# Performance work log

Measured on AMD Instinct MI355X. Metric: run time of the kernel, lower is better.

## Reference

```python
import jax, jax.numpy as jnp
import numpy as np
import math

CHUNK = 32
NS_STEPS = 5
MAX_GNORM = 10.0


def _normalize(x, eps=1e-12):
    n = jnp.linalg.norm(x, axis=-1, keepdims=True)
    return x / jnp.maximum(n, eps)


def _poly(x):  # poly_degree = 2: [x, x^2] / sqrt(2)
    return jnp.concatenate([x, x * x], axis=-1) / math.sqrt(2.0)


def _ns5(G):
    # Muon-style Newton-Schulz orthogonalization (quintic, 5 steps)
    a, b, c = 3.4445, -4.7750, 2.0315
    t = G.shape[0] > G.shape[1]
    X = G.T if t else G
    X = X / (jnp.linalg.norm(X) + 1e-7)
    for _ in range(NS_STEPS):
        A = X @ X.T
        B = b * A + c * (A @ A)
        X = a * X + B @ X
    return X.T if t else X


def _clip_mean(g):
    # per-sample grad-norm clipping to MAX_GNORM, then mean over samples
    n = g.shape[0]
    norms = jnp.maximum(jnp.linalg.norm(g.reshape(n, -1), axis=1), 1e-8)
    scale = jnp.maximum(norms / MAX_GNORM, 1.0)
    return jnp.mean(g / scale.reshape((n,) + (1,) * (g.ndim - 1)), axis=0)


def _mem_fwd(W0, W1, z):  # MemoryMLP depth=2, gelu (exact) between layers
    return jax.nn.gelu(z @ W0, approximate=False) @ W1


def setup_inputs() -> dict:
    key = jax.random.key(0)
    ks = jax.random.split(key, 16)
    B, S, D, M, P, H = 2, 1024, 2048, 512, 1024, 2048
    w = lambda k, shape, fan_in: jax.random.normal(k, shape, jnp.float32) / np.float32(np.sqrt(fan_in))
    return {
        "x": jax.random.normal(ks[0], (B, S, D), jnp.float32),
        "Wk": w(ks[1], (M, D), D),
        "Wv": w(ks[2], (M, D), D),
        "Wq": w(ks[3], (M, D), D),
        "Wout": w(ks[4], (D, M), M),
        "w_lr": w(ks[5], (1, D), D), "b_lr": jnp.full((1,), -4.0, jnp.float32),
        "w_mom": w(ks[6], (1, D), D), "b_mom": jnp.full((1,), 1.0, jnp.float32),
        "w_dec": w(ks[7], (1, D), D), "b_dec": jnp.full((1,), -3.0, jnp.float32),
        "w_gate": w(ks[8], (1, D), D), "b_gate": jnp.full((1,), -1.0, jnp.float32),
        "Wmem0": w(ks[9], (P, H), P),
        "Wmem1": w(ks[10], (H, P), H),
        "Wmemout": w(ks[11], (P, M), P),
        "Wvexp": w(ks[12], (M, P), M),
    }


def reference(x, Wk, Wv, Wq, Wout, w_lr, b_lr, w_mom, b_mom, w_dec, b_dec,
              w_gate, b_gate, Wmem0, Wmem1, Wmemout, Wvexp):
    # Inference path (torch.is_grad_enabled() == False): chunked ATLAS update.
    B, S, D = x.shape
    NC = S // CHUNK

    k = _normalize(x @ Wk.T)          # (B,S,M)
    v = x @ Wv.T                       # (B,S,M)
    q = _normalize(x @ Wq.T)          # (B,S,M)
    kp = _poly(k)                      # (B,S,P)
    qp = _poly(q)                      # (B,S,P)
    vexp = v @ Wvexp                   # v_expand: (B,S,P)

    gate = lambda w, b: jax.nn.sigmoid(jnp.einsum('bsd,od->bso', x, w) + b)
    lr, mom, dec, og = gate(w_lr, b_lr), gate(w_mom, b_mom), gate(w_dec, b_dec), gate(w_gate, b_gate)

    cmean = lambda t: t[..., 0].reshape(B, NC, CHUNK).mean(axis=(0, 2))  # per-chunk scalar
    lr_c, mom_c, dec_c = cmean(lr), cmean(mom), cmean(dec)

    chunks = lambda t: t.reshape(B, NC, CHUNK, t.shape[-1]).transpose(1, 0, 2, 3)  # (NC,B,C,F)
    qc, kc, vc = chunks(qp), chunks(kp), chunks(vexp)

    def loss_fn(params, kk, vv):  # ||M(k) - v||^2 per sample
        W0_, W1_ = params
        pred = jax.nn.gelu(kk @ W0_, approximate=False) @ W1_
        return jnp.sum((pred - vv) ** 2)

    grad_fn = jax.vmap(jax.grad(loss_fn), in_axes=((None, None), 0, 0))

    def step(carry, xs):
        W0, W1, S0, S1 = carry
        qch, kch, vch, lrc, momc, decc = xs
        retr = _mem_fwd(W0, W1, qch) @ Wmemout  # retrieve with pre-update params: (B,C,M)
        kf = kch.reshape(-1, kch.shape[-1])
        vf = vch.reshape(-1, vch.shape[-1])
        g0, g1 = grad_fn((W0, W1), kf, vf)      # per-sample grads
        g0, g1 = _clip_mean(g0), _clip_mean(g1)
        s0 = momc * S0 - lrc * g0                # surprise momentum
        s1 = momc * S1 - lrc * g1
        W0n = (1.0 - decc) * W0 + _ns5(s0) * lrc # forget gate + orthogonalized step
        W1n = (1.0 - decc) * W1 + _ns5(s1) * lrc
        return (W0n, W1n, s0, s1), retr

    init = (Wmem0, Wmem1, jnp.zeros_like(Wmem0), jnp.zeros_like(Wmem1))
    _, retrs = jax.lax.scan(step, init, (qc, kc, vc, lr_c, mom_c, dec_c))
    retrieved = retrs.transpose(1, 0, 2, 3).reshape(B, S, -1)  # (B,S,M)
    delta = retrieved @ Wout.T
    return x + delta * og
```

## Files before the change

kernel.cpp:

```cpp
#include <hip/hip_runtime.h>


typedef unsigned short us;
typedef __attribute__((ext_vector_type(8))) short s16x8;
typedef __attribute__((ext_vector_type(8))) unsigned short u16x8;
typedef __attribute__((ext_vector_type(4))) float f32x4;

#define MKP 72

__device__ __forceinline__ float gelu_f(float x) {
  return 0.5f * x * (1.0f + erff(x * 0.70710678118654752f));
}
__device__ __forceinline__ float gelu_grad_f(float x) {
  float cdf = 0.5f * (1.0f + erff(x * 0.70710678118654752f));
  float pdf = 0.3989422804014327f * expf(-0.5f * x * x);
  return cdf + x * pdf;
}
__device__ __forceinline__ float sigmoid_f(float x) { return 1.0f / (1.0f + expf(-x)); }

__device__ __forceinline__ us f2bf(float f) {
  union { float f; unsigned u; } v; v.f = f;
  unsigned r = (v.u + 0x7FFFu + ((v.u >> 16) & 1u)) >> 16;
  return (us)r;
}
__device__ __forceinline__ float bf2f(us h) {
  union { unsigned u; float f; } v; v.u = ((unsigned)h) << 16;
  return v.f;
}
__device__ __forceinline__ int cm_map(int n) {
  return ((n & 1023) >> 5) * 64 + (n >> 10) * 32 + (n & 31);
}

__device__ __forceinline__ float block_reduce_sum(float v, float* red) {
  int t = threadIdx.x;
  red[t] = v; __syncthreads();
  for (int s = blockDim.x >> 1; s > 0; s >>= 1) {
    if (t < s) red[t] += red[t + s];
    __syncthreads();
  }
  float r = red[0];
  __syncthreads();
  return r;
}

template<int EPI, int TA, int DUAL, int AG>
__global__ __launch_bounds__(64)
void mg_k(const us* __restrict__ Aq, const us* __restrict__ A2,
          const us* __restrict__ Bq, void* __restrict__ Cq,
          void* __restrict__ C2, const void* __restrict__ Eq,
          const float* __restrict__ FX, const float* __restrict__ OG,
          const float* __restrict__ cp, int cidx,
          int M, int N, int K, int lda, int ldb, int ldc, int lde,
          float c1, float c2, long sA, long sB, long sC, long sE) {
  __shared__ __align__(16) us As[64 * MKP];
  __shared__ __align__(16) us Bs[64 * MKP];
  const int bz = blockIdx.z;
  const us* A = Aq + (size_t)bz * sA;
  const us* B = Bq + (size_t)bz * sB;
  const int t = threadIdx.x;
  const int m0 = blockIdx.y * 64, n0 = blockIdx.x * 64;
  if constexpr (DUAL) { if (m0 >= 64) A = A2; }
  const int mA0 = DUAL ? (m0 & 63) : m0;
  const int l15 = t & 15, l4 = t >> 4;

  f32x4 acc[4][4];
#pragma unroll
  for (int i = 0; i < 4; ++i)
#pragma unroll
    for (int j = 0; j < 4; ++j) acc[i][j] = (f32x4){0.f, 0.f, 0.f, 0.f};

  const int srw = t >> 3;
  const int sck = (t & 7) * 8;

  u16x8 ra[8], rb[8];
  auto LDA = [&](int k0) {
#pragma unroll
    for (int p = 0; p < 8; ++p) {
      if constexpr (TA == 0) {
        int row = srw + p * 8;
        int srow;
        if constexpr (AG) srow = cm_map(m0 + row); else srow = mA0 + row;
        ra[p] = *(const u16x8*)(A + (size_t)srow * lda + k0 + sck);
      } else {
        ra[p] = *(const u16x8*)(A + (size_t)(k0 + srw + p * 8) * lda + mA0 + sck);
      }
    }
  };
  auto LDB = [&](int k0) {
#pragma unroll
    for (int p = 0; p < 8; ++p)
      rb[p] = *(const u16x8*)(B + (size_t)(n0 + srw + p * 8) * ldb + k0 + sck);
  };

  LDA(0); LDB(0);
  for (int k0 = 0; k0 < K; k0 += 64) {
    if constexpr (TA == 0) {
#pragma unroll
      for (int p = 0; p < 8; ++p)
        *(u16x8*)&As[(srw + p * 8) * MKP + sck] = ra[p];
    } else {
#pragma unroll
      for (int p = 0; p < 8; ++p) {
        int kk = srw + p * 8;
#pragma unroll
        for (int j = 0; j < 8; ++j) As[(sck + j) * MKP + kk] = ra[p][j];
      }
    }
#pragma unroll
    for (int p = 0; p < 8; ++p)
      *(u16x8*)&Bs[(srw + p * 8) * MKP + sck] = rb[p];
    if (k0 + 64 < K) { LDA(k0 + 64); LDB(k0 + 64); }
#pragma unroll
    for (int ks = 0; ks < 2; ++ks) {
      s16x8 af[4], bf[4];
#pragma unroll
      for (int mi = 0; mi < 4; ++mi)
        af[mi] = *(const s16x8*)&As[(mi * 16 + l15) * MKP + ks * 32 + l4 * 8];
#pragma unroll
      for (int ni = 0; ni < 4; ++ni)
        bf[ni] = *(const s16x8*)&Bs[(ni * 16 + l15) * MKP + ks * 32 + l4 * 8];
#pragma unroll
      for (int mi = 0; mi < 4; ++mi)
#pragma unroll
        for (int ni = 0; ni < 4; ++ni)
          acc[mi][ni] = __builtin_amdgcn_mfma_f32_16x16x32_bf16(af[mi], bf[ni], acc[mi][ni], 0, 0, 0);
    }
  }

#pragma unroll
  for (int mi = 0; mi < 4; ++mi) {
#pragma unroll
    for (int i = 0; i < 4; ++i) {
      int grow = m0 + mi * 16 + l4 * 4 + i;
#pragma unroll
      for (int ni = 0; ni < 4; ++ni) {
        int col = n0 + ni * 16 + l15;
        float v = acc[mi][ni][i];
        if constexpr (EPI == 5) {
          ((us*)Cq + bz * sC)[(size_t)grow * ldc + col] = f2bf(v);
        } else if constexpr (EPI == 6) {
          const us* E = (const us*)Eq + bz * sE;
          ((us*)Cq + bz * sC)[(size_t)grow * ldc + col] =
              f2bf(c1 * v + c2 * bf2f(E[(size_t)grow * lde + col]));
        } else if constexpr (EPI == 7) {
          ((float*)Cq)[(size_t)grow * ldc + col] = v;
        } else if constexpr (EPI == 8) {
          ((us*)Cq)[(size_t)grow * ldc + col] = f2bf(gelu_f(v));
          if (m0 >= 64)
            ((float*)C2)[(size_t)(grow - 64) * ldc + col] = gelu_grad_f(v);
        } else if constexpr (EPI == 9) {
          if (m0 < 64)
            ((us*)Cq)[(size_t)grow * ldc + col] = f2bf(v);
          else
            ((us*)Cq)[(size_t)grow * ldc + col] =
                f2bf(2.0f * (v - ((const float*)Eq)[(size_t)(grow - 64) * lde + col]));
        } else if constexpr (EPI == 13) {
          ((float*)Cq)[(size_t)grow * ldc + col] =
              v * ((const float*)Eq)[(size_t)grow * lde + col];
        } else if constexpr (EPI == 14) {
          float* C = (float*)Cq;
          float old = C[(size_t)grow * ldc + col];
          C[(size_t)grow * ldc + col] = cp[cidx * 3 + 1] * old - cp[cidx * 3 + 0] * v;
        } else if constexpr (EPI == 15) {
          ((float*)Cq)[(size_t)grow * ldc + col] =
              FX[(size_t)grow * ldc + col] + v * OG[grow];
        } else if constexpr (EPI == 17) {
          int crow = cm_map(grow);
          ((float*)Cq)[(size_t)crow * ldc + col] = v;
        }
      }
    }
  }
}

template<int EPI, int TA = 0, int DUAL = 0, int AG = 0>
static void mg(hipStream_t st, const us* A, const us* A2, const us* B,
               void* C, void* C2, const void* E,
               const float* FX, const float* OG, const float* cp, int cidx,
               int M, int N, int K, int lda, int ldb, int ldc, int lde,
               float c1, float c2, long sA, long sB, long sC, long sE, int batch) {
  dim3 g(N / 64, M / 64, batch), b(64);
  hipLaunchKernelGGL((mg_k<EPI, TA, DUAL, AG>), g, b, 0, st, A, A2, B, C, C2, E,
                     FX, OG, cp, cidx, M, N, K, lda, ldb, ldc, lde, c1, c2, sA, sB, sC, sE);
}


__global__ __launch_bounds__(256) void conv_k(const float* __restrict__ in,
                                              us* __restrict__ out, int n) {
  for (int i = blockIdx.x * 256 + threadIdx.x; i < n; i += gridDim.x * 256)
    out[i] = f2bf(in[i]);
}

__global__ void tconv_k(const float* __restrict__ in, us* __restrict__ out, int R, int C) {
  __shared__ float tile[32][33];
  int c0 = blockIdx.x * 32, r0 = blockIdx.y * 32;
  int tx = threadIdx.x, ty = threadIdx.y;
#pragma unroll
  for (int j = 0; j < 4; ++j)
    tile[ty + 8 * j][tx] = in[(size_t)(r0 + ty + 8 * j) * C + c0 + tx];
  __syncthreads();
#pragma unroll
  for (int j = 0; j < 4; ++j)
    out[(size_t)(c0 + ty + 8 * j) * R + r0 + tx] = f2bf(tile[tx][ty + 8 * j]);
}


__global__ __launch_bounds__(256) void polynorm2_k(const float* __restrict__ lin,
                                                   us* __restrict__ outp) {
  __shared__ float red[256];
  int n = blockIdx.x, t = threadIdx.x;
  int rowp = cm_map(n);
  float s = 0.f;
  for (int f = t; f < 512; f += 256) { float v = lin[(size_t)n * 512 + f]; s += v * v; }
  float tot = block_reduce_sum(s, red);
  float sc = 1.0f / fmaxf(sqrtf(tot), 1e-12f);
  const float is2 = 0.70710678118654752f;
  for (int f = t; f < 512; f += 256) {
    float v = lin[(size_t)n * 512 + f] * sc;
    outp[(size_t)rowp * 1024 + f] = f2bf(v * is2);
    outp[(size_t)rowp * 1024 + 512 + f] = f2bf(v * v * is2);
  }
}

__global__ __launch_bounds__(256) void gates_k(const float* __restrict__ x,
    const float* __restrict__ wlr, const float* __restrict__ blr,
    const float* __restrict__ wmom, const float* __restrict__ bmom,
    const float* __restrict__ wdec, const float* __restrict__ bdec,
    const float* __restrict__ wgate, const float* __restrict__ bgate,
    float* __restrict__ lrv, float* __restrict__ momv,
    float* __restrict__ decv, float* __restrict__ og) {
  __shared__ float red[256];
  int n = blockIdx.x, t = threadIdx.x;
  float s0 = 0.f, s1 = 0.f, s2 = 0.f, s3 = 0.f;
  for (int d = t; d < 2048; d += 256) {
    float xv = x[(size_t)n * 2048 + d];
    s0 += xv * wlr[d]; s1 += xv * wmom[d]; s2 += xv * wdec[d]; s3 += xv * wgate[d];
  }
  float r0 = block_reduce_sum(s0, red);
  float r1 = block_reduce_sum(s1, red);
  float r2 = block_reduce_sum(s2, red);
  float r3 = block_reduce_sum(s3, red);
  if (t == 0) {
    lrv[n] = sigmoid_f(r0 + blr[0]);
    momv[n] = sigmoid_f(r1 + bmom[0]);
    decv[n] = sigmoid_f(r2 + bdec[0]);
    og[n] = sigmoid_f(r3 + bgate[0]);
  }
}

__global__ void chunk_means_k(const float* __restrict__ lrv, const float* __restrict__ momv,
                              const float* __restrict__ decv, float* __restrict__ cp) {
  int c = blockIdx.x, t = threadIdx.x;
  int n = ((t >> 5) << 10) + c * 32 + (t & 31);
  float a = lrv[n], b = momv[n], d = decv[n];
  for (int off = 32; off > 0; off >>= 1) {
    a += __shfl_down(a, off);
    b += __shfl_down(b, off);
    d += __shfl_down(d, off);
  }
  if (t == 0) {
    cp[c * 3 + 0] = a * (1.f / 64.f);
    cp[c * 3 + 1] = b * (1.f / 64.f);
    cp[c * 3 + 2] = d * (1.f / 64.f);
  }
}

__global__ __launch_bounds__(256) void sampnorm2_k(const us* __restrict__ kp_b,
                                                   const float* __restrict__ dh,
                                                   const us* __restrict__ hab,
                                                   const us* __restrict__ pr,
                                                   float* __restrict__ w0inv,
                                                   float* __restrict__ w1inv, int c) {
  __shared__ float red[256];
  int i = blockIdx.x, t = threadIdx.x;
  int row = c * 64 + i;
  float sk = 0.f, sr = 0.f, sdh = 0.f, sa = 0.f;
  for (int p = t; p < 1024; p += 256) {
    float v = bf2f(kp_b[(size_t)row * 1024 + p]); sk += v * v;
    v = bf2f(pr[(size_t)(64 + i) * 1024 + p]); sr += v * v;
  }
  for (int h = t; h < 2048; h += 256) {
    float v = dh[(size_t)i * 2048 + h]; sdh += v * v;
    v = bf2f(hab[(size_t)(64 + i) * 2048 + h]); sa += v * v;
  }
  float tk = block_reduce_sum(sk, red);
  float tdh = block_reduce_sum(sdh, red);
  float ta = block_reduce_sum(sa, red);
  float tr = block_reduce_sum(sr, red);
  if (t == 0) {
    float n0 = fmaxf(sqrtf(tk) * sqrtf(tdh), 1e-8f);
    w0inv[i] = 1.0f / (64.0f * fmaxf(n0 * 0.1f, 1.0f));
    float n1 = fmaxf(sqrtf(ta) * sqrtf(tr), 1e-8f);
    w1inv[i] = 1.0f / (64.0f * fmaxf(n1 * 0.1f, 1.0f));
  }
}

template<int INF32>
__global__ void wtrans_k(const void* __restrict__ in, const float* __restrict__ w,
                         us* __restrict__ out, int C, int ldin) {
  __shared__ float tile[32][33];
  int c0 = blockIdx.x * 32, r0 = blockIdx.y * 32;
  int tx = threadIdx.x, ty = threadIdx.y;
#pragma unroll
  for (int j = 0; j < 4; ++j) {
    int r = r0 + ty + 8 * j, cc = c0 + tx;
    float v;
    if constexpr (INF32) v = ((const float*)in)[(size_t)r * ldin + cc];
    else v = bf2f(((const us*)in)[(size_t)r * ldin + cc]);
    tile[ty + 8 * j][tx] = v * w[r];
  }
  __syncthreads();
#pragma unroll
  for (int j = 0; j < 4; ++j)
    out[(size_t)(c0 + ty + 8 * j) * 64 + r0 + tx] = f2bf(tile[tx][ty + 8 * j]);
}

__global__ __launch_bounds__(256) void frob2_k(const float* __restrict__ s0,
                                               const float* __restrict__ s1, int n,
                                               float* __restrict__ parts) {
  __shared__ float red[256];
  const float* s = blockIdx.z ? s1 : s0;
  float acc = 0.f;
  for (int i = blockIdx.x * 256 + threadIdx.x; i < n; i += gridDim.x * 256) {
    float v = s[i]; acc += v * v;
  }
  float r = block_reduce_sum(acc, red);
  if (threadIdx.x == 0) parts[blockIdx.z * 256 + blockIdx.x] = r;
}

__global__ __launch_bounds__(256) void frob_fin2_k(const float* __restrict__ parts,
                                                   float* __restrict__ inv) {
  __shared__ float red[256];
  float r = block_reduce_sum(parts[blockIdx.x * 256 + threadIdx.x], red);
  if (threadIdx.x == 0) inv[blockIdx.x] = 1.0f / (sqrtf(r) + 1e-7f);
}

__global__ void scale_dual_k(const float* __restrict__ in, us* __restrict__ outS,
                             us* __restrict__ outT, const float* __restrict__ inv,
                             int R, int C) {
  __shared__ float tile[32][33];
  float s = *inv;
  int c0 = blockIdx.x * 32, r0 = blockIdx.y * 32;
  int tx = threadIdx.x, ty = threadIdx.y;
#pragma unroll
  for (int j = 0; j < 4; ++j) {
    float v = in[(size_t)(r0 + ty + 8 * j) * C + c0 + tx];
    tile[ty + 8 * j][tx] = v;
    outS[(size_t)(r0 + ty + 8 * j) * C + c0 + tx] = f2bf(v * s);
  }
  __syncthreads();
#pragma unroll
  for (int j = 0; j < 4; ++j)
    outT[(size_t)(c0 + ty + 8 * j) * R + r0 + tx] = f2bf(tile[tx][ty + 8 * j] * s);
}

__global__ void tbf_k(const us* __restrict__ in, us* __restrict__ out) {
  __shared__ us tile[32][33];
  size_t bo = (size_t)blockIdx.z * 2097152;
  int c0 = blockIdx.x * 32, r0 = blockIdx.y * 32;
  int tx = threadIdx.x, ty = threadIdx.y;
#pragma unroll
  for (int j = 0; j < 4; ++j)
    tile[ty + 8 * j][tx] = in[bo + (size_t)(r0 + ty + 8 * j) * 2048 + c0 + tx];
  __syncthreads();
#pragma unroll
  for (int j = 0; j < 4; ++j)
    out[bo + (size_t)(c0 + ty + 8 * j) * 1024 + r0 + tx] = tile[tx][ty + 8 * j];
}

__global__ void wupd0_k(float* __restrict__ W0, const us* __restrict__ X,
                        us* __restrict__ W0bT, const float* __restrict__ cp, int c) {
  __shared__ float tl[32][33];
  float lr = cp[c * 3 + 0], om = 1.0f - cp[c * 3 + 2];
  int c0 = blockIdx.x * 32, r0 = blockIdx.y * 32;
  int tx = threadIdx.x, ty = threadIdx.y;
#pragma unroll
  for (int j = 0; j < 4; ++j) {
    int r = r0 + ty + 8 * j, h = c0 + tx;
    size_t idx = (size_t)r * 2048 + h;
    float v = om * W0[idx] + lr * bf2f(X[idx]);
    W0[idx] = v;
    tl[ty + 8 * j][tx] = v;
  }
  __syncthreads();
#pragma unroll
  for (int j = 0; j < 4; ++j)
    W0bT[(size_t)(c0 + ty + 8 * j) * 1024 + r0 + tx] = f2bf(tl[tx][ty + 8 * j]);
}

__global__ void wupd1_k(float* __restrict__ W1, const us* __restrict__ X2,
                        us* __restrict__ W1b, us* __restrict__ W1bT,
                        const float* __restrict__ cp, int c) {
  __shared__ float tX[32][33];
  __shared__ float t2[32][33];
  float lr = cp[c * 3 + 0], om = 1.0f - cp[c * 3 + 2];
  int h0 = blockIdx.x * 32, p0 = blockIdx.y * 32;
  int tx = threadIdx.x, ty = threadIdx.y;
#pragma unroll
  for (int j = 0; j < 4; ++j)
    tX[ty + 8 * j][tx] = bf2f(X2[(size_t)(p0 + ty + 8 * j) * 2048 + h0 + tx]);
  __syncthreads();
#pragma unroll
  for (int j = 0; j < 4; ++j) {
    int h = h0 + ty + 8 * j, p = p0 + tx;
    size_t idx = (size_t)h * 1024 + p;
    float v = om * W1[idx] + lr * tX[tx][ty + 8 * j];
    W1[idx] = v;
    W1b[idx] = f2bf(v);
    t2[tx][ty + 8 * j] = v;
  }
  __syncthreads();
#pragma unroll
  for (int j = 0; j < 4; ++j)
    W1bT[(size_t)(p0 + ty + 8 * j) * 2048 + h0 + tx] = f2bf(t2[ty + 8 * j][tx]);
}


extern "C" void kernel_launch(void* const* d_in, const int* in_sizes, int n_in,
                              void* d_out, int out_size, void* d_ws, size_t ws_size,
                              hipStream_t stream) {
  const float* x = (const float*)d_in[0];
  const float* Wk = (const float*)d_in[1];
  const float* Wv = (const float*)d_in[2];
  const float* Wq = (const float*)d_in[3];
  const float* Wout = (const float*)d_in[4];
  const float* w_lr = (const float*)d_in[5];
  const float* b_lr = (const float*)d_in[6];
  const float* w_mom = (const float*)d_in[7];
  const float* b_mom = (const float*)d_in[8];
  const float* w_dec = (const float*)d_in[9];
  const float* b_dec = (const float*)d_in[10];
  const float* w_gate = (const float*)d_in[11];
  const float* b_gate = (const float*)d_in[12];
  const float* Wmem0 = (const float*)d_in[13];
  const float* Wmem1 = (const float*)d_in[14];
  const float* Wmemout = (const float*)d_in[15];
  const float* Wvexp = (const float*)d_in[16];
  float* out = (float*)d_out;
  (void)n_in; (void)in_sizes; (void)out_size;

  const long F = 1048576;
  const long BIG = 2097152;
  const long SB2 = 2097152, SB1 = 1048576;
  float* ws = (float*)d_ws;
  if (ws_size < (size_t)25043464 * sizeof(float)) return;

  us* kp_b   = (us*)ws;
  us* qp_b   = (us*)(ws + F);
  float* vexp = ws + 2 * F;
  float* W0  = ws + 4 * F;
  float* W1  = ws + 6 * F;
  float* S0  = ws + 8 * F;
  float* S1  = ws + 10 * F;
  us* XA     = (us*)(ws + 12 * F);
  us* XB     = (us*)(ws + 14 * F);
  us* XT     = (us*)(ws + 16 * F);
  us* Ab     = (us*)(ws + 18 * F);
  float* SCR = ws + 19 * F;
  us* W0bT   = (us*)(ws + 20 * F);
  us* W1bT   = (us*)(ws + 21 * F);
  us* W1b    = (us*)(ws + 22 * F);
  us* WmoT   = (us*)(ws + 23 * F);
  us* retrv  = (us*)(ws + 23 * F + 262144);
  float* smal = ws + 23 * F + 262144 + 524288;
  float* og   = smal;
  float* lrv  = og + 2048;
  float* momv = lrv + 2048;
  float* decv = momv + 2048;
  float* cpb  = decv + 2048;
  float* w0inv = cpb + 128;
  float* w1inv = w0inv + 64;
  float* parts = w1inv + 64;
  float* inv01 = parts + 512;

  us* xb   = XA;
  us* Wkb  = XB;
  us* Wqb  = XB + 1048576;
  us* Wvb  = XB + 2097152;
  us* vlin = XT;
  us* WvexpT = XT + 1048576;
  us* Woutb = Ab;
  float* lin = SCR;
  us* Bb = (us*)SCR;
  us* hab   = (us*)SCR;
  float* gp = SCR + 131072;
  us* pr    = (us*)(SCR + 262144);
  float* dh = SCR + 327680;
  us* dhT   = (us*)(SCR + 458752);
  us* rbwT  = (us*)(SCR + 524288);

  const float NSa = 3.4445f, NSb = -4.7750f, NSc = 2.0315f;

  hipMemcpyAsync(W0, Wmem0, (size_t)BIG * 4, hipMemcpyDeviceToDevice, stream);
  hipMemcpyAsync(W1, Wmem1, (size_t)BIG * 4, hipMemcpyDeviceToDevice, stream);
  hipMemsetAsync(S0, 0, (size_t)BIG * 4, stream);
  hipMemsetAsync(S1, 0, (size_t)BIG * 4, stream);
  hipLaunchKernelGGL(tconv_k, dim3(64, 32), dim3(32, 8), 0, stream, Wmem0, W0bT, 1024, 2048);
  hipLaunchKernelGGL(conv_k, dim3(1024), dim3(256), 0, stream, Wmem1, W1b, (int)BIG);
  hipLaunchKernelGGL(tconv_k, dim3(32, 64), dim3(32, 8), 0, stream, Wmem1, W1bT, 2048, 1024);
  hipLaunchKernelGGL(tconv_k, dim3(16, 32), dim3(32, 8), 0, stream, Wmemout, WmoT, 1024, 512);
  hipLaunchKernelGGL(tconv_k, dim3(32, 16), dim3(32, 8), 0, stream, Wvexp, WvexpT, 512, 1024);
  hipLaunchKernelGGL(conv_k, dim3(2048), dim3(256), 0, stream, x, xb, 2048 * 2048);
  hipLaunchKernelGGL(conv_k, dim3(512), dim3(256), 0, stream, Wk, Wkb, 512 * 2048);
  hipLaunchKernelGGL(conv_k, dim3(512), dim3(256), 0, stream, Wq, Wqb, 512 * 2048);
  hipLaunchKernelGGL(conv_k, dim3(512), dim3(256), 0, stream, Wv, Wvb, 512 * 2048);

  mg<7>(stream, xb, nullptr, Wkb, lin, nullptr, nullptr, nullptr, nullptr, nullptr, 0,
        2048, 512, 2048, 2048, 2048, 512, 0, 0.f, 0.f, 0, 0, 0, 0, 1);
  hipLaunchKernelGGL(polynorm2_k, dim3(2048), dim3(256), 0, stream, lin, kp_b);
  mg<7>(stream, xb, nullptr, Wqb, lin, nullptr, nullptr, nullptr, nullptr, nullptr, 0,
        2048, 512, 2048, 2048, 2048, 512, 0, 0.f, 0.f, 0, 0, 0, 0, 1);
  hipLaunchKernelGGL(polynorm2_k, dim3(2048), dim3(256), 0, stream, lin, qp_b);
  mg<5>(stream, xb, nullptr, Wvb, vlin, nullptr, nullptr, nullptr, nullptr, nullptr, 0,
        2048, 512, 2048, 2048, 2048, 512, 0, 0.f, 0.f, 0, 0, 0, 0, 1);
  mg<17>(stream, vlin, nullptr, WvexpT, vexp, nullptr, nullptr, nullptr, nullptr, nullptr, 0,
         2048, 1024, 512, 512, 512, 1024, 0, 0.f, 0.f, 0, 0, 0, 0, 1);

  hipLaunchKernelGGL(gates_k, dim3(2048), dim3(256), 0, stream, x,
                     w_lr, b_lr, w_mom, b_mom, w_dec, b_dec, w_gate, b_gate,
                     lrv, momv, decv, og);
  hipLaunchKernelGGL(chunk_means_k, dim3(32), dim3(64), 0, stream, lrv, momv, decv, cpb);

  for (int c = 0; c < 32; ++c) {
    const us* kp_c = kp_b + (size_t)c * 64 * 1024;
    const us* qp_c = qp_b + (size_t)c * 64 * 1024;
    const float* vexp_c = vexp + (size_t)c * 64 * 1024;
    mg<8, 0, 1>(stream, qp_c, kp_c, W0bT, hab, gp, nullptr, nullptr, nullptr, nullptr, 0,
                128, 2048, 1024, 1024, 1024, 2048, 0, 0.f, 0.f, 0, 0, 0, 0, 1);
    mg<9>(stream, hab, nullptr, W1bT, pr, nullptr, vexp_c, nullptr, nullptr, nullptr, 0,
          128, 1024, 2048, 2048, 2048, 1024, 1024, 0.f, 0.f, 0, 0, 0, 0, 1);
    mg<5>(stream, pr, nullptr, WmoT, retrv + (size_t)c * 64 * 512, nullptr, nullptr,
          nullptr, nullptr, nullptr, 0,
          64, 512, 1024, 1024, 1024, 512, 0, 0.f, 0.f, 0, 0, 0, 0, 1);
    mg<13>(stream, pr + 64 * 1024, nullptr, W1b, dh, nullptr, gp, nullptr, nullptr, nullptr, 0,
           64, 2048, 1024, 1024, 1024, 2048, 2048, 0.f, 0.f, 0, 0, 0, 0, 1);
    hipLaunchKernelGGL(sampnorm2_k, dim3(64), dim3(256), 0, stream,
                       kp_b, dh, hab, pr, w0inv, w1inv, c);
    hipLaunchKernelGGL((wtrans_k<1>), dim3(64, 2), dim3(32, 8), 0, stream, dh, w0inv, dhT, 2048, 2048);
    hipLaunchKernelGGL((wtrans_k<0>), dim3(32, 2), dim3(32, 8), 0, stream, pr + 64 * 1024, w1inv,
                       rbwT, 1024, 1024);
    mg<14, 1>(stream, kp_c, nullptr, dhT, S0, nullptr, nullptr, nullptr, nullptr, cpb, c,
              1024, 2048, 64, 1024, 64, 2048, 0, 0.f, 0.f, 0, 0, 0, 0, 1);
    mg<14, 1>(stream, hab + 64 * 2048, nullptr, rbwT, S1, nullptr, nullptr, nullptr, nullptr, cpb, c,
              2048, 1024, 64, 2048, 64, 1024, 0, 0.f, 0.f, 0, 0, 0, 0, 1);

    hipLaunchKernelGGL(frob2_k, dim3(256, 1, 2), dim3(256), 0, stream, S0, S1, (int)BIG, parts);
    hipLaunchKernelGGL(frob_fin2_k, dim3(2), dim3(256), 0, stream, parts, inv01);
    hipLaunchKernelGGL(scale_dual_k, dim3(64, 32), dim3(32, 8), 0, stream,
                       S0, XA, XT, inv01, 1024, 2048);
    hipLaunchKernelGGL(scale_dual_k, dim3(32, 64), dim3(32, 8), 0, stream,
                       S1, XT + SB2, XA + SB2, inv01 + 1, 2048, 1024);

    us* Xc = XA;
    us* Xn = XB;
    for (int it = 0; it < 5; ++it) {
      mg<5>(stream, Xc, nullptr, Xc, Ab, nullptr, nullptr, nullptr, nullptr, nullptr, 0,
            1024, 1024, 2048, 2048, 2048, 1024, 0, 0.f, 0.f, SB2, SB2, SB1, 0, 2);
      mg<6>(stream, Ab, nullptr, Ab, Bb, nullptr, Ab, nullptr, nullptr, nullptr, 0,
            1024, 1024, 1024, 1024, 1024, 1024, 1024, NSc, NSb, SB1, SB1, SB1, SB1, 2);
      mg<6>(stream, Bb, nullptr, XT, Xn, nullptr, Xc, nullptr, nullptr, nullptr, 0,
            1024, 2048, 1024, 1024, 1024, 2048, 2048, 1.0f, NSa, SB1, SB2, SB2, SB2, 2);
      if (it < 4)
        hipLaunchKernelGGL(tbf_k, dim3(64, 32, 2), dim3(32, 8), 0, stream, Xn, XT);
      us* tmp = Xc; Xc = Xn; Xn = tmp;
    }
    hipLaunchKernelGGL(wupd0_k, dim3(64, 32), dim3(32, 8), 0, stream, W0, Xc, W0bT, cpb, c);
    hipLaunchKernelGGL(wupd1_k, dim3(64, 32), dim3(32, 8), 0, stream, W1, Xc + SB2, W1b, W1bT, cpb, c);
  }

  hipLaunchKernelGGL(conv_k, dim3(1024), dim3(256), 0, stream, Wout, Woutb, 2048 * 512);
  mg<15, 0, 0, 1>(stream, retrv, nullptr, Woutb, out, nullptr, nullptr, x, og, nullptr, 0,
                  2048, 2048, 512, 512, 512, 2048, 0, 0.f, 0.f, 0, 0, 0, 0, 1);
}
```

Baseline: 16.89 ms.

## Use 128x128 LDS-direct GEMM with split-K for Newton-Schulz iterations

Adds a new 256-thread GEMM kernel with 128x128 tiles, swizzled shared memory and direct global-to-LDS loads, and uses it for the three Newton-Schulz matmuls. The two square products (X X^T and A A) are split along K into two partial results, which are then summed by small elementwise combine kernels. This is meant to raise occupancy on the 1024x1024 outputs and improve data reuse compared with the 64x64 single-wave kernel. In exchange it adds extra kernel launches and memory traffic for the partials, and bf16 partial sums add rounding error.

```diff
diff --git a/kernel.cpp b/kernel.cpp
--- a/kernel.cpp
+++ b/kernel.cpp
@@ -29,6 +29,12 @@
 }
 __device__ __forceinline__ int cm_map(int n) {
   return ((n & 1023) >> 5) * 64 + (n >> 10) * 32 + (n & 31);
+}
+
+__device__ __forceinline__ void gload16(const us* g, us* l) {
+  __builtin_amdgcn_global_load_lds(
+      (const __attribute__((address_space(1))) void*)g,
+      (__attribute__((address_space(3))) void*)l, 16, 0, 0);
 }
 
 __device__ __forceinline__ float block_reduce_sum(float v, float* red) {
@@ -41,6 +47,125 @@
   float r = red[0];
   __syncthreads();
   return r;
+}
+
+template<int KS, int EPI>
+__global__ __launch_bounds__(256)
+void ns_k(const us* __restrict__ Aq, const us* __restrict__ Bq,
+          us* __restrict__ Cq, const us* __restrict__ Eq,
+          int M, int N, int K, int lda, int ldb, int ldc, int lde,
+          float c1, float c2, long sA, long sB, long sC, long sE) {
+  __shared__ __align__(16) us As[128 * 64];
+  __shared__ __align__(16) us Bs[128 * 64];
+  const int bz = blockIdx.z;
+  const int bb = bz / KS, ss = bz % KS;
+  const int KH = K / KS;
+  const us* A = Aq + (size_t)bb * sA + (size_t)ss * KH;
+  const us* B = Bq + (size_t)bb * sB + (size_t)ss * KH;
+  us* C = Cq + (size_t)bz * sC;
+  const int t = threadIdx.x;
+  const int wave = t >> 6, lane = t & 63;
+  const int m0 = blockIdx.y * 128, n0 = blockIdx.x * 128;
+  const int wm = (wave >> 1) * 64, wn = (wave & 1) * 64;
+  const int l15 = lane & 15, l4 = lane >> 4;
+  const int lr = lane >> 3;
+  const int lu = lane & 7;
+
+  f32x4 acc[4][4];
+#pragma unroll
+  for (int i = 0; i < 4; ++i)
+#pragma unroll
+    for (int j = 0; j < 4; ++j) acc[i][j] = (f32x4){0.f, 0.f, 0.f, 0.f};
+
+  for (int k0 = 0; k0 < KH; k0 += 64) {
+#pragma unroll
+    for (int j = 0; j < 4; ++j) {
+      int r = (wave * 4 + j) * 8 + lr;
+      int u = lu ^ (r & 7);
+      gload16(A + (size_t)(m0 + r) * lda + k0 + u * 8, As + (wave * 4 + j) * 512);
+      gload16(B + (size_t)(n0 + r) * ldb + k0 + u * 8, Bs + (wave * 4 + j) * 512);
+    }
+    __syncthreads();
+#pragma unroll
+    for (int ks = 0; ks < 2; ++ks) {
+      s16x8 af[4], bf[4];
+#pragma unroll
+      for (int mi = 0; mi < 4; ++mi) {
+        int ra = wm + mi * 16 + l15;
+        int cu = (ks * 4 + l4) ^ (ra & 7);
+        af[mi] = *(const s16x8*)&As[ra * 64 + cu * 8];
+      }
+#pragma unroll
+      for (int ni = 0; ni < 4; ++ni) {
+        int rb = wn + ni * 16 + l15;
+        int cu = (ks * 4 + l4) ^ (rb & 7);
+        bf[ni] = *(const s16x8*)&Bs[rb * 64 + cu * 8];
+      }
+#pragma unroll
+      for (int mi = 0; mi < 4; ++mi)
+#pragma unroll
+        for (int ni = 0; ni < 4; ++ni)
+          acc[mi][ni] = __builtin_amdgcn_mfma_f32_16x16x32_bf16(af[mi], bf[ni], acc[mi][ni], 0, 0, 0);
+    }
+    __syncthreads();
+  }
+
+#pragma unroll
+  for (int mi = 0; mi < 4; ++mi) {
+#pragma unroll
+    for (int i = 0; i < 4; ++i) {
+      int row = m0 + wm + mi * 16 + l4 * 4 + i;
+#pragma unroll
+      for (int ni = 0; ni < 4; ++ni) {
+        int col = n0 + wn + ni * 16 + l15;
+        float v = acc[mi][ni][i];
+        if constexpr (EPI == 0) {
+          C[(size_t)row * ldc + col] = f2bf(v);
+        } else {
+          const us* E = Eq + (size_t)bb * sE;
+          C[(size_t)row * ldc + col] =
+              f2bf(c1 * v + c2 * bf2f(E[(size_t)row * lde + col]));
+        }
+      }
+    }
+  }
+}
+
+template<int KS, int EPI>
+static void nsg(hipStream_t st, const us* A, const us* B, us* C, const us* E,
+                int M, int N, int K, int lda, int ldb, int ldc, int lde,
+                float c1, float c2, long sA, long sB, long sC, long sE, int batch) {
+  dim3 g(N / 128, M / 128, batch * KS), b(256);
+  hipLaunchKernelGGL((ns_k<KS, EPI>), g, b, 0, st, A, B, C, E,
+                     M, N, K, lda, ldb, ldc, lde, c1, c2, sA, sB, sC, sE);
+}
+
+__global__ __launch_bounds__(256) void combA_k(const u16x8* __restrict__ P,
+                                               u16x8* __restrict__ Ab) {
+  int i = blockIdx.x * 256 + threadIdx.x;
+  int b = i >> 17, j = i & 131071;
+  u16x8 p0 = P[(size_t)(b * 2) * 131072 + j];
+  u16x8 p1 = P[(size_t)(b * 2 + 1) * 131072 + j];
+  u16x8 o;
+#pragma unroll
+  for (int q = 0; q < 8; ++q) o[q] = f2bf(bf2f(p0[q]) + bf2f(p1[q]));
+  Ab[i] = o;
+}
+
+__global__ __launch_bounds__(256) void combB_k(const u16x8* __restrict__ P,
+                                               const u16x8* __restrict__ Ab,
+                                               u16x8* __restrict__ Bb,
+                                               float nsb, float nsc) {
+  int i = blockIdx.x * 256 + threadIdx.x;
+  int b = i >> 17, j = i & 131071;
+  u16x8 p0 = P[(size_t)(b * 2) * 131072 + j];
+  u16x8 p1 = P[(size_t)(b * 2 + 1) * 131072 + j];
+  u16x8 ab = Ab[i];
+  u16x8 o;
+#pragma unroll
+  for (int q = 0; q < 8; ++q)
+    o[q] = f2bf(nsc * (bf2f(p0[q]) + bf2f(p1[q])) + nsb * bf2f(ab[q]));
+  Bb[i] = o;
 }
 
 template<int EPI, int TA, int DUAL, int AG>
@@ -138,10 +263,6 @@
         float v = acc[mi][ni][i];
         if constexpr (EPI == 5) {
           ((us*)Cq + bz * sC)[(size_t)grow * ldc + col] = f2bf(v);
-        } else if constexpr (EPI == 6) {
-          const us* E = (const us*)Eq + bz * sE;
-          ((us*)Cq + bz * sC)[(size_t)grow * ldc + col] =
-              f2bf(c1 * v + c2 * bf2f(E[(size_t)grow * lde + col]));
         } else if constexpr (EPI == 7) {
           ((float*)Cq)[(size_t)grow * ldc + col] = v;
         } else if constexpr (EPI == 8) {
@@ -554,12 +675,17 @@
     us* Xc = XA;
     us* Xn = XB;
     for (int it = 0; it < 5; ++it) {
-      mg<5>(stream, Xc, nullptr, Xc, Ab, nullptr, nullptr, nullptr, nullptr, nullptr, 0,
-            1024, 1024, 2048, 2048, 2048, 1024, 0, 0.f, 0.f, SB2, SB2, SB1, 0, 2);
-      mg<6>(stream, Ab, nullptr, Ab, Bb, nullptr, Ab, nullptr, nullptr, nullptr, 0,
-            1024, 1024, 1024, 1024, 1024, 1024, 1024, NSc, NSb, SB1, SB1, SB1, SB1, 2);
-      mg<6>(stream, Bb, nullptr, XT, Xn, nullptr, Xc, nullptr, nullptr, nullptr, 0,
-            1024, 2048, 1024, 1024, 1024, 2048, 2048, 1.0f, NSa, SB1, SB2, SB2, SB2, 2);
+      us* P = Xn;
+      nsg<2, 0>(stream, Xc, Xc, P, nullptr, 1024, 1024, 2048, 2048, 2048, 1024, 0,
+                0.f, 0.f, SB2, SB2, SB1, 0, 2);
+      hipLaunchKernelGGL(combA_k, dim3(1024), dim3(256), 0, stream,
+                         (const u16x8*)P, (u16x8*)Ab);
+      nsg<2, 0>(stream, Ab, Ab, P, nullptr, 1024, 1024, 1024, 1024, 1024, 1024, 0,
+                0.f, 0.f, SB1, SB1, SB1, 0, 2);
+      hipLaunchKernelGGL(combB_k, dim3(1024), dim3(256), 0, stream,
+                         (const u16x8*)P, (const u16x8*)Ab, (u16x8*)Bb, NSb, NSc);
+      nsg<1, 6>(stream, Bb, XT, Xn, Xc, 1024, 2048, 1024, 1024, 1024, 2048, 2048,
+                1.0f, NSa, SB1, SB2, SB2, SB2, 2);
       if (it < 4)
         hipLaunchKernelGGL(tbf_k, dim3(64, 32, 2), dim3(32, 8), 0, stream, Xn, XT);
       us* tmp = Xc; Xc = Xn; Xn = tmp;
```

After: 17.79 ms. 1.05x slower.

## Split-K the Newton-Schulz GEMMs and fuse combine with transpose

Applied to the files above, without the earlier changes.

Each of the three Newton-Schulz GEMMs per iteration is split into two K halves, doubling the block count to improve CU occupancy on the small 64-thread-block grid. The partial bf16 results are summed by new combine kernels that also apply the polynomial coefficients. The final combine fuses the transpose previously done by tbf_k. This adds extra partial-sum traffic and kernel launches, reuses scratch buffers such as W0bT, and rounds the partials to bf16 before summing, which slightly changes precision.

```diff
diff --git a/kernel.cpp b/kernel.cpp
--- a/kernel.cpp
+++ b/kernel.cpp
@@ -43,90 +43,11 @@
   return r;
 }
 
-template<int EPI, int TA, int DUAL, int AG>
-__global__ __launch_bounds__(64)
-void mg_k(const us* __restrict__ Aq, const us* __restrict__ A2,
-          const us* __restrict__ Bq, void* __restrict__ Cq,
-          void* __restrict__ C2, const void* __restrict__ Eq,
-          const float* __restrict__ FX, const float* __restrict__ OG,
-          const float* __restrict__ cp, int cidx,
-          int M, int N, int K, int lda, int ldb, int ldc, int lde,
-          float c1, float c2, long sA, long sB, long sC, long sE) {
-  __shared__ __align__(16) us As[64 * MKP];
-  __shared__ __align__(16) us Bs[64 * MKP];
-  const int bz = blockIdx.z;
-  const us* A = Aq + (size_t)bz * sA;
-  const us* B = Bq + (size_t)bz * sB;
-  const int t = threadIdx.x;
-  const int m0 = blockIdx.y * 64, n0 = blockIdx.x * 64;
-  if constexpr (DUAL) { if (m0 >= 64) A = A2; }
-  const int mA0 = DUAL ? (m0 & 63) : m0;
-  const int l15 = t & 15, l4 = t >> 4;
-
-  f32x4 acc[4][4];
-#pragma unroll
-  for (int i = 0; i < 4; ++i)
-#pragma unroll
-    for (int j = 0; j < 4; ++j) acc[i][j] = (f32x4){0.f, 0.f, 0.f, 0.f};
-
-  const int srw = t >> 3;
-  const int sck = (t & 7) * 8;
-
-  u16x8 ra[8], rb[8];
-  auto LDA = [&](int k0) {
-#pragma unroll
-    for (int p = 0; p < 8; ++p) {
-      if constexpr (TA == 0) {
-        int row = srw + p * 8;
-        int srow;
-        if constexpr (AG) srow = cm_map(m0 + row); else srow = mA0 + row;
-        ra[p] = *(const u16x8*)(A + (size_t)srow * lda + k0 + sck);
-      } else {
-        ra[p] = *(const u16x8*)(A + (size_t)(k0 + srw + p * 8) * lda + mA0 + sck);
-      }
-    }
-  };
-  auto LDB = [&](int k0) {
-#pragma unroll
-    for (int p = 0; p < 8; ++p)
-      rb[p] = *(const u16x8*)(B + (size_t)(n0 + srw + p * 8) * ldb + k0 + sck);
-  };
-
-  LDA(0); LDB(0);
-  for (int k0 = 0; k0 < K; k0 += 64) {
-    if constexpr (TA == 0) {
-#pragma unroll
-      for (int p = 0; p < 8; ++p)
-        *(u16x8*)&As[(srw + p * 8) * MKP + sck] = ra[p];
-    } else {
-#pragma unroll
-      for (int p = 0; p < 8; ++p) {
-        int kk = srw + p * 8;
-#pragma unroll
-        for (int j = 0; j < 8; ++j) As[(sck + j) * MKP + kk] = ra[p][j];
-      }
-    }
-#pragma unroll
-    for (int p = 0; p < 8; ++p)
-      *(u16x8*)&Bs[(srw + p * 8) * MKP + sck] = rb[p];
-    if (k0 + 64 < K) { LDA(k0 + 64); LDB(k0 + 64); }
-#pragma unroll
-    for (int ks = 0; ks < 2; ++ks) {
-      s16x8 af[4], bf[4];
-#pragma unroll
-      for (int mi = 0; mi < 4; ++mi)
-        af[mi] = *(const s16x8*)&As[(mi * 16 + l15) * MKP + ks * 32 + l4 * 8];
-#pragma unroll
-      for (int ni = 0; ni < 4; ++ni)
-        bf[ni] = *(const s16x8*)&Bs[(ni * 16 + l15) * MKP + ks * 32 + l4 * 8];
-#pragma unroll
-      for (int mi = 0; mi < 4; ++mi)
-#pragma unroll
-        for (int ni = 0; ni < 4; ++ni)
-          acc[mi][ni] = __builtin_amdgcn_mfma_f32_16x16x32_bf16(af[mi], bf[ni], acc[mi][ni], 0, 0, 0);
-    }
-  }
-
+template<int EPI>
+__device__ __forceinline__ void epilogue(f32x4 (&acc)[4][4], int m0, int n0,
+    int l15, int l4, void* Cq, void* C2, const void* Eq,
+    const float* FX, const float* OG, const float* cp, int cidx,
+    int ldc, int lde, float c1, float c2) {
 #pragma unroll
   for (int mi = 0; mi < 4; ++mi) {
 #pragma unroll
@@ -137,11 +58,10 @@
         int col = n0 + ni * 16 + l15;
         float v = acc[mi][ni][i];
         if constexpr (EPI == 5) {
-          ((us*)Cq + bz * sC)[(size_t)grow * ldc + col] = f2bf(v);
+          ((us*)Cq)[(size_t)grow * ldc + col] = f2bf(v);
         } else if constexpr (EPI == 6) {
-          const us* E = (const us*)Eq + bz * sE;
-          ((us*)Cq + bz * sC)[(size_t)grow * ldc + col] =
-              f2bf(c1 * v + c2 * bf2f(E[(size_t)grow * lde + col]));
+          ((us*)Cq)[(size_t)grow * ldc + col] =
+              f2bf(c1 * v + c2 * bf2f(((const us*)Eq)[(size_t)grow * lde + col]));
         } else if constexpr (EPI == 7) {
           ((float*)Cq)[(size_t)grow * ldc + col] = v;
         } else if constexpr (EPI == 8) {
@@ -173,15 +93,176 @@
   }
 }
 
-template<int EPI, int TA = 0, int DUAL = 0, int AG = 0>
+template<int EPI, int TA, int DUAL, int AG, int KS>
+__global__ __launch_bounds__(64)
+void mg_k(const us* __restrict__ Aq, const us* __restrict__ A2,
+          const us* __restrict__ Bq, void* __restrict__ Cq,
+          void* __restrict__ C2, const void* __restrict__ Eq,
+          const float* __restrict__ FX, const float* __restrict__ OG,
+          const float* __restrict__ cp, int cidx,
+          int M, int N, int K, int lda, int ldb, int ldc, int lde,
+          float c1, float c2, long sA, long sB, long sC, long sE, int zthr) {
+  __shared__ __align__(16) us As[64 * MKP];
+  __shared__ __align__(16) us Bs[64 * MKP];
+  const int bz = blockIdx.z;
+  const int bb = bz / KS, ss = bz % KS;
+  const int KH = K / KS;
+  const us* A = Aq + (size_t)bb * sA;
+  if constexpr (TA == 0) A += (size_t)ss * KH;
+  else A += (size_t)ss * KH * lda;
+  const us* B = Bq + (size_t)bb * sB + (size_t)ss * KH;
+  const int t = threadIdx.x;
+  const int m0 = blockIdx.y * 64, n0 = blockIdx.x * 64;
+  if constexpr (DUAL) { if (m0 >= 64) A = A2; }
+  const int mA0 = DUAL ? (m0 & 63) : m0;
+  const int l15 = t & 15, l4 = t >> 4;
+
+  f32x4 acc[4][4];
+#pragma unroll
+  for (int i = 0; i < 4; ++i)
+#pragma unroll
+    for (int j = 0; j < 4; ++j) acc[i][j] = (f32x4){0.f, 0.f, 0.f, 0.f};
+
+  const int srw = t >> 3;
+  const int sck = (t & 7) * 8;
+
+  u16x8 ra[8], rb[8];
+  auto LDA = [&](int k0) {
+#pragma unroll
+    for (int p = 0; p < 8; ++p) {
+      if constexpr (TA == 0) {
+        int row = srw + p * 8;
+        int srow;
+        if constexpr (AG) srow = cm_map(m0 + row); else srow = mA0 + row;
+        ra[p] = *(const u16x8*)(A + (size_t)srow * lda + k0 + sck);
+      } else {
+        ra[p] = *(const u16x8*)(A + (size_t)(k0 + srw + p * 8) * lda + mA0 + sck);
+      }
+    }
+  };
+  auto LDB = [&](int k0) {
+#pragma unroll
+    for (int p = 0; p < 8; ++p)
+      rb[p] = *(const u16x8*)(B + (size_t)(n0 + srw + p * 8) * ldb + k0 + sck);
+  };
+
+  LDA(0); LDB(0);
+  for (int k0 = 0; k0 < KH; k0 += 64) {
+    if constexpr (TA == 0) {
+#pragma unroll
+      for (int p = 0; p < 8; ++p)
+        *(u16x8*)&As[(srw + p * 8) * MKP + sck] = ra[p];
+    } else {
+#pragma unroll
+      for (int p = 0; p < 8; ++p) {
+        int kk = srw + p * 8;
+#pragma unroll
+        for (int j = 0; j < 8; ++j) As[(sck + j) * MKP + kk] = ra[p][j];
+      }
+    }
+#pragma unroll
+    for (int p = 0; p < 8; ++p)
+      *(u16x8*)&Bs[(srw + p * 8) * MKP + sck] = rb[p];
+    if (k0 + 64 < KH) { LDA(k0 + 64); LDB(k0 + 64); }
+#pragma unroll
+    for (int ks = 0; ks < 2; ++ks) {
+      s16x8 af[4], bf[4];
+#pragma unroll
+      for (int mi = 0; mi < 4; ++mi)
+        af[mi] = *(const s16x8*)&As[(mi * 16 + l15) * MKP + ks * 32 + l4 * 8];
+#pragma unroll
+      for (int ni = 0; ni < 4; ++ni)
+        bf[ni] = *(const s16x8*)&Bs[(ni * 16 + l15) * MKP + ks * 32 + l4 * 8];
+#pragma unroll
+      for (int mi = 0; mi < 4; ++mi)
+#pragma unroll
+        for (int ni = 0; ni < 4; ++ni)
+          acc[mi][ni] = __builtin_amdgcn_mfma_f32_16x16x32_bf16(af[mi], bf[ni], acc[mi][ni], 0, 0, 0);
+    }
+  }
+
+  if constexpr (EPI == 5 || EPI == 6) {
+    void* Cb; long cb;
+    if (bz < zthr) { Cb = Cq; cb = bz; } else { Cb = C2; cb = bz - zthr; }
+    us* Cp = (us*)Cb + (size_t)cb * sC;
+    const us* Ep = (const us*)Eq + (size_t)bb * sE;
+    epilogue<EPI>(acc, m0, n0, l15, l4, Cp, nullptr, Ep, FX, OG, cp, cidx,
+                  ldc, lde, c1, c2);
+  } else {
+    epilogue<EPI>(acc, m0, n0, l15, l4, Cq, C2, Eq, FX, OG, cp, cidx,
+                  ldc, lde, c1, c2);
+  }
+}
+
+template<int EPI, int TA = 0, int DUAL = 0, int AG = 0, int KS = 1>
 static void mg(hipStream_t st, const us* A, const us* A2, const us* B,
                void* C, void* C2, const void* E,
                const float* FX, const float* OG, const float* cp, int cidx,
                int M, int N, int K, int lda, int ldb, int ldc, int lde,
-               float c1, float c2, long sA, long sB, long sC, long sE, int batch) {
-  dim3 g(N / 64, M / 64, batch), b(64);
-  hipLaunchKernelGGL((mg_k<EPI, TA, DUAL, AG>), g, b, 0, st, A, A2, B, C, C2, E,
-                     FX, OG, cp, cidx, M, N, K, lda, ldb, ldc, lde, c1, c2, sA, sB, sC, sE);
+               float c1, float c2, long sA, long sB, long sC, long sE,
+               int batch, int zthr = (1 << 30)) {
+  dim3 g(N / 64, M / 64, batch * KS), b(64);
+  hipLaunchKernelGGL((mg_k<EPI, TA, DUAL, AG, KS>), g, b, 0, st, A, A2, B, C, C2, E,
+                     FX, OG, cp, cidx, M, N, K, lda, ldb, ldc, lde, c1, c2,
+                     sA, sB, sC, sE, zthr);
+}
+
+
+__global__ __launch_bounds__(256) void combA_k(const u16x8* __restrict__ P,
+                                               u16x8* __restrict__ Ab) {
+  int i = blockIdx.x * 256 + threadIdx.x;
+  int b = i >> 17, j = i & 131071;
+  u16x8 p0 = P[(size_t)(b * 2) * 131072 + j];
+  u16x8 p1 = P[(size_t)(b * 2 + 1) * 131072 + j];
+  u16x8 o;
+#pragma unroll
+  for (int q = 0; q < 8; ++q) o[q] = f2bf(bf2f(p0[q]) + bf2f(p1[q]));
+  Ab[i] = o;
+}
+
+__global__ __launch_bounds__(256) void combB_k(const u16x8* __restrict__ P,
+                                               const u16x8* __restrict__ Ab,
+                                               u16x8* __restrict__ Bb,
+                                               float nsb, float nsc) {
+  int i = blockIdx.x * 256 + threadIdx.x;
+  int b = i >> 17, j = i & 131071;
+  u16x8 p0 = P[(size_t)(b * 2) * 131072 + j];
+  u16x8 p1 = P[(size_t)(b * 2 + 1) * 131072 + j];
+  u16x8 ab = Ab[i];
+  u16x8 o;
+#pragma unroll
+  for (int q = 0; q < 8; ++q)
+    o[q] = f2bf(nsc * (bf2f(p0[q]) + bf2f(p1[q])) + nsb * bf2f(ab[q]));
+  Bb[i] = o;
+}
+
+__global__ void combX_k(const us* __restrict__ P0, const us* __restrict__ P1,
+                        const us* __restrict__ Xc, us* __restrict__ Xn,
+                        us* __restrict__ XT, float nsa, int doT) {
+  __shared__ us tile[32][33];
+  const long SB2c = 2097152;
+  int b = blockIdx.z;
+  int h0 = blockIdx.x * 32, r0 = blockIdx.y * 32;
+  int tx = threadIdx.x, ty = threadIdx.y;
+  const us* pa = (b * 2 == 0) ? P0 : P1 + (size_t)(b * 2 - 1) * SB2c;
+  const us* pb = P1 + (size_t)(b * 2) * SB2c;
+  const us* xc = Xc + (size_t)b * SB2c;
+  us* xn = Xn + (size_t)b * SB2c;
+  us* xt = XT + (size_t)b * SB2c;
+#pragma unroll
+  for (int j = 0; j < 4; ++j) {
+    size_t idx = (size_t)(r0 + ty + 8 * j) * 2048 + h0 + tx;
+    float v = bf2f(pa[idx]) + bf2f(pb[idx]) + nsa * bf2f(xc[idx]);
+    us uv = f2bf(v);
+    xn[idx] = uv;
+    tile[ty + 8 * j][tx] = uv;
+  }
+  __syncthreads();
+  if (doT) {
+#pragma unroll
+    for (int j = 0; j < 4; ++j)
+      xt[(size_t)(h0 + ty + 8 * j) * 1024 + r0 + tx] = tile[tx][ty + 8 * j];
+  }
 }
 
 
@@ -352,20 +433,6 @@
 #pragma unroll
   for (int j = 0; j < 4; ++j)
     outT[(size_t)(c0 + ty + 8 * j) * R + r0 + tx] = f2bf(tile[tx][ty + 8 * j] * s);
-}
-
-__global__ void tbf_k(const us* __restrict__ in, us* __restrict__ out) {
-  __shared__ us tile[32][33];
-  size_t bo = (size_t)blockIdx.z * 2097152;
-  int c0 = blockIdx.x * 32, r0 = blockIdx.y * 32;
-  int tx = threadIdx.x, ty = threadIdx.y;
-#pragma unroll
-  for (int j = 0; j < 4; ++j)
-    tile[ty + 8 * j][tx] = in[bo + (size_t)(r0 + ty + 8 * j) * 2048 + c0 + tx];
-  __syncthreads();
-#pragma unroll
-  for (int j = 0; j < 4; ++j)
-    out[bo + (size_t)(c0 + ty + 8 * j) * 1024 + r0 + tx] = tile[tx][ty + 8 * j];
 }
 
 __global__ void wupd0_k(float* __restrict__ W0, const us* __restrict__ X,
@@ -554,14 +621,25 @@
     us* Xc = XA;
     us* Xn = XB;
     for (int it = 0; it < 5; ++it) {
-      mg<5>(stream, Xc, nullptr, Xc, Ab, nullptr, nullptr, nullptr, nullptr, nullptr, 0,
-            1024, 1024, 2048, 2048, 2048, 1024, 0, 0.f, 0.f, SB2, SB2, SB1, 0, 2);
-      mg<6>(stream, Ab, nullptr, Ab, Bb, nullptr, Ab, nullptr, nullptr, nullptr, 0,
-            1024, 1024, 1024, 1024, 1024, 1024, 1024, NSc, NSb, SB1, SB1, SB1, SB1, 2);
-      mg<6>(stream, Bb, nullptr, XT, Xn, nullptr, Xc, nullptr, nullptr, nullptr, 0,
-            1024, 2048, 1024, 1024, 1024, 2048, 2048, 1.0f, NSa, SB1, SB2, SB2, SB2, 2);
-      if (it < 4)
-        hipLaunchKernelGGL(tbf_k, dim3(64, 32, 2), dim3(32, 8), 0, stream, Xn, XT);
+      us* P = Xn;
+      mg<5, 0, 0, 0, 2>(stream, Xc, nullptr, Xc, P, nullptr, nullptr,
+                        nullptr, nullptr, nullptr, 0,
+                        1024, 1024, 2048, 2048, 2048, 1024, 0, 0.f, 0.f,
+                        SB2, SB2, SB1, 0, 2);
+      hipLaunchKernelGGL(combA_k, dim3(1024), dim3(256), 0, stream,
+                         (const u16x8*)P, (u16x8*)Ab);
+      mg<5, 0, 0, 0, 2>(stream, Ab, nullptr, Ab, P, nullptr, nullptr,
+                        nullptr, nullptr, nullptr, 0,
+                        1024, 1024, 1024, 1024, 1024, 1024, 0, 0.f, 0.f,
+                        SB1, SB1, SB1, 0, 2);
+      hipLaunchKernelGGL(combB_k, dim3(1024), dim3(256), 0, stream,
+                         (const u16x8*)P, (const u16x8*)Ab, (u16x8*)Bb, NSb, NSc);
+      mg<5, 0, 0, 0, 2>(stream, Bb, nullptr, XT, Ab, W0bT, nullptr,
+                        nullptr, nullptr, nullptr, 0,
+                        1024, 2048, 1024, 1024, 1024, 2048, 0, 0.f, 0.f,
+                        SB1, SB2, SB2, 0, 2, 1);
+      hipLaunchKernelGGL(combX_k, dim3(64, 32, 2), dim3(32, 8), 0, stream,
+                         Ab, W0bT, Xc, Xn, XT, NSa, it < 4 ? 1 : 0);
       us* tmp = Xc; Xc = Xn; Xn = tmp;
     }
     hipLaunchKernelGGL(wupd0_k, dim3(64, 32), dim3(32, 8), 0, stream, W0, Xc, W0bT, cpb, c);
```

Measured after the change: 17.23 ms. +2.0%, slower.
